# Kernel tuning notes

Hardware: AMD Instinct MI355X
Metric: run time of the kernel (lower is better)

Reference implementation:

```python
import jax, jax.numpy as jnp
import numpy as np

N = 50000          # nodes
E = 800000         # directed edges (avg degree 16)
IN_F = 1433        # Cora num_features
N_CLS = 7          # Cora num_classes
HEADS = 8
HID = 32
NEG_SLOPE = 0.2    # PyG GATConv default negative_slope


def gat_conv(x, src, dst, W, a_src, a_dst, bias, heads, out_ch):
    """PyG GATConv (concat=True, add_self_loops=True, eval mode)."""
    n = x.shape[0]
    h = (x @ W).reshape(n, heads, out_ch)            # [N, H, C]
    # add self loops (PyG default)
    loop = jnp.arange(n, dtype=src.dtype)
    src = jnp.concatenate([src, loop])
    dst = jnp.concatenate([dst, loop])
    # attention logits per edge: a_src . h_src + a_dst . h_dst
    alpha_src = (h * a_src).sum(-1)                  # [N, H]
    alpha_dst = (h * a_dst).sum(-1)                  # [N, H]
    e = jax.nn.leaky_relu(alpha_src[src] + alpha_dst[dst], NEG_SLOPE)  # [E+N, H]
    # segment softmax over incoming edges of each destination node
    m = jax.ops.segment_max(e, dst, num_segments=n)  # [N, H]
    p = jnp.exp(e - m[dst])
    denom = jax.ops.segment_sum(p, dst, num_segments=n)
    alpha = p / denom[dst]                           # [E+N, H]
    # attention-weighted scatter-aggregate of source features
    out = jax.ops.segment_sum(h[src] * alpha[:, :, None], dst, num_segments=n)  # [N, H, C]
    return out.reshape(n, heads * out_ch) + bias


def setup_inputs() -> dict:
    key = jax.random.key(0)
    ks = jax.random.split(key, 12)
    s = 0.05
    x = jax.random.normal(ks[0], (N, IN_F), dtype=jnp.float32)
    edge_index = jax.random.randint(ks[1], (2, E), 0, N, dtype=jnp.int32)
    W1 = jax.random.normal(ks[2], (IN_F, HEADS * HID), dtype=jnp.float32) * s
    att_src1 = jax.random.normal(ks[3], (HEADS, HID), dtype=jnp.float32) * s
    att_dst1 = jax.random.normal(ks[4], (HEADS, HID), dtype=jnp.float32) * s
    bias1 = jnp.zeros((HEADS * HID,), dtype=jnp.float32)
    W2 = jax.random.normal(ks[5], (HEADS * HID, HEADS * N_CLS), dtype=jnp.float32) * s
    att_src2 = jax.random.normal(ks[6], (HEADS, N_CLS), dtype=jnp.float32) * s
    att_dst2 = jax.random.normal(ks[7], (HEADS, N_CLS), dtype=jnp.float32) * s
    bias2 = jnp.zeros((HEADS * N_CLS,), dtype=jnp.float32)
    return {
        "x": x, "edge_index": edge_index,
        "W1": W1, "att_src1": att_src1, "att_dst1": att_dst1, "bias1": bias1,
        "W2": W2, "att_src2": att_src2, "att_dst2": att_dst2, "bias2": bias2,
    }


def reference(x, edge_index, W1, att_src1, att_dst1, bias1,
              W2, att_src2, att_dst2, bias2):
    src, dst = edge_index[0], edge_index[1]
    # dropout (p=0.6) is identity in eval mode
    h = gat_conv(x, src, dst, W1, att_src1, att_dst1, bias1, HEADS, HID)
    h = jax.nn.elu(h)
    out = gat_conv(h, src, dst, W2, att_src2, att_dst2, bias2, HEADS, N_CLS)
    return out  # [N, HEADS * N_CLS]
```

## Files before the change

### kernel.cpp

```cpp
#include <hip/hip_runtime.h>
#include <math.h>

typedef short s16x8 __attribute__((ext_vector_type(8)));
typedef float f32x4 __attribute__((ext_vector_type(4)));

#define SLOPE 0.2f
#define K1 1433
#define KP 1440
#define NKB 45

static __device__ __forceinline__ float leaky(float x) {
  return x > 0.f ? x : SLOPE * x;
}

static __device__ __forceinline__ unsigned short f2bf(float f) {
  unsigned u = __builtin_bit_cast(unsigned, f);
  u += 0x7FFFu + ((u >> 16) & 1u);
  return (unsigned short)(u >> 16);
}
static __device__ __forceinline__ float bf2f(unsigned short h) {
  unsigned u = ((unsigned)h) << 16;
  return __builtin_bit_cast(float, u);
}

__global__ void w1t_kernel(const float* __restrict__ W1,
                           unsigned short* __restrict__ w1f) {
  int tid = blockIdx.x * 256 + threadIdx.x;
  if (tid >= NKB * 2 * 16 * 64) return;
  int l = tid & 63;
  int chunk = tid >> 6;
  int ntg = chunk & 15;
  int hl = (chunk >> 4) & 1;
  int kb = chunk >> 5;
  int n = ntg * 16 + (l & 15);
  int kbase = kb * 32 + (l >> 4) * 8;
  unsigned short o[8];
#pragma unroll
  for (int e = 0; e < 8; ++e) {
    int k = kbase + e;
    float v = (k < K1) ? W1[(long)k * 256 + n] : 0.f;
    unsigned short h = f2bf(v);
    o[e] = hl ? f2bf(v - bf2f(h)) : h;
  }
  *(ulonglong2*)(w1f + (long)tid * 8) = *(ulonglong2*)o;
}

__global__ __launch_bounds__(256) void gemm1_mfma_kernel(
    const float* __restrict__ A, const unsigned short* __restrict__ w1f,
    float* __restrict__ C, int M) {
  __shared__ unsigned short As[2][4 * 2 * 64 * 8];
  __shared__ unsigned short Bs[2][16 * 2 * 64 * 8];
  const int t = threadIdx.x;
  const int w = t >> 6, l = t & 63;
  const int row0 = blockIdx.x * 64;

  f32x4 acc[4][4];
#pragma unroll
  for (int mt = 0; mt < 4; ++mt)
#pragma unroll
    for (int nt = 0; nt < 4; ++nt)
#pragma unroll
      for (int r = 0; r < 4; ++r) acc[mt][nt][r] = 0.f;

  const int sr = t >> 2, sg = t & 3;
  const int smt = sr >> 4, slr = sr & 15;
  const int lane_dst = slr + 16 * sg;
  const bool rowok = (row0 + sr) < M;
  const float* arow = A + (long)(row0 + sr) * K1;

  float v[8];

#pragma unroll
  for (int q = 0; q < 8; ++q) {
    int c = w * 8 + q, ng = c >> 1, hl = c & 1;
    const unsigned short* gsrc = w1f + ((((long)0 * 2 + hl) * 16 + ng) * 64 + l) * 8;
    unsigned short* ldst = &Bs[0][(ng * 2 + hl) * 512];
    __builtin_amdgcn_global_load_lds(
        (const __attribute__((address_space(1))) unsigned int*)gsrc,
        (__attribute__((address_space(3))) unsigned int*)ldst, 16, 0, 0);
  }
  {
    int kbase = sg * 8;
#pragma unroll
    for (int i = 0; i < 8; ++i) {
      int gk = kbase + i;
      v[i] = (rowok && gk < K1) ? arow[gk] : 0.f;
    }
    unsigned short hv[8], lv[8];
#pragma unroll
    for (int e = 0; e < 8; ++e) {
      unsigned short h = f2bf(v[e]);
      hv[e] = h;
      lv[e] = f2bf(v[e] - bf2f(h));
    }
    *(ulonglong2*)&As[0][((smt * 2 + 0) * 64 + lane_dst) * 8] = *(ulonglong2*)hv;
    *(ulonglong2*)&As[0][((smt * 2 + 1) * 64 + lane_dst) * 8] = *(ulonglong2*)lv;
  }
  __syncthreads();

  int cur = 0;
  for (int kb = 0; kb < NKB; ++kb) {
    const int nxt = kb + 1;
    if (nxt < NKB) {
#pragma unroll
      for (int q = 0; q < 8; ++q) {
        int c = w * 8 + q, ng = c >> 1, hl = c & 1;
        const unsigned short* gsrc =
            w1f + ((((long)nxt * 2 + hl) * 16 + ng) * 64 + l) * 8;
        unsigned short* ldst = &Bs[cur ^ 1][(ng * 2 + hl) * 512];
        __builtin_amdgcn_global_load_lds(
            (const __attribute__((address_space(1))) unsigned int*)gsrc,
            (__attribute__((address_space(3))) unsigned int*)ldst, 16, 0, 0);
      }
      int kbase = nxt * 32 + sg * 8;
#pragma unroll
      for (int i = 0; i < 8; ++i) {
        int gk = kbase + i;
        v[i] = (rowok && gk < K1) ? arow[gk] : 0.f;
      }
    }
    {
      s16x8 ah[4], al[4];
#pragma unroll
      for (int mt = 0; mt < 4; ++mt) {
        ah[mt] = *(const s16x8*)&As[cur][(mt * 2 + 0) * 512 + l * 8];
        al[mt] = *(const s16x8*)&As[cur][(mt * 2 + 1) * 512 + l * 8];
      }
#pragma unroll
      for (int nt = 0; nt < 4; ++nt) {
        int ng = w * 4 + nt;
        s16x8 bh = *(const s16x8*)&Bs[cur][(ng * 2 + 0) * 512 + l * 8];
        s16x8 bl = *(const s16x8*)&Bs[cur][(ng * 2 + 1) * 512 + l * 8];
#pragma unroll
        for (int mt = 0; mt < 4; ++mt) {
          acc[mt][nt] = __builtin_amdgcn_mfma_f32_16x16x32_bf16(
              ah[mt], bh, acc[mt][nt], 0, 0, 0);
          acc[mt][nt] = __builtin_amdgcn_mfma_f32_16x16x32_bf16(
              ah[mt], bl, acc[mt][nt], 0, 0, 0);
          acc[mt][nt] = __builtin_amdgcn_mfma_f32_16x16x32_bf16(
              al[mt], bh, acc[mt][nt], 0, 0, 0);
        }
      }
    }
    if (nxt < NKB) {
      unsigned short hv[8], lv[8];
#pragma unroll
      for (int e = 0; e < 8; ++e) {
        unsigned short h = f2bf(v[e]);
        hv[e] = h;
        lv[e] = f2bf(v[e] - bf2f(h));
      }
      *(ulonglong2*)&As[cur ^ 1][((smt * 2 + 0) * 64 + lane_dst) * 8] =
          *(ulonglong2*)hv;
      *(ulonglong2*)&As[cur ^ 1][((smt * 2 + 1) * 64 + lane_dst) * 8] =
          *(ulonglong2*)lv;
      __syncthreads();
    }
    cur ^= 1;
  }
  const int crow4 = (l >> 4) * 4;
  const int ccol = l & 15;
#pragma unroll
  for (int mt = 0; mt < 4; ++mt) {
#pragma unroll
    for (int r = 0; r < 4; ++r) {
      int grow = row0 + mt * 16 + crow4 + r;
      if (grow < M) {
#pragma unroll
        for (int nt = 0; nt < 4; ++nt) {
          int gcol = w * 64 + nt * 16 + ccol;
          C[(long)grow * 256 + gcol] = acc[mt][nt][r];
        }
      }
    }
  }
}

__global__ void alpha1_kernel(const float* __restrict__ h1,
    const float* __restrict__ a_src, const float* __restrict__ a_dst,
    float* __restrict__ as_o, float* __restrict__ ad_o, int N) {
  int i = blockIdx.x * blockDim.x + threadIdx.x;
  if (i >= N * 8) return;
  int h = i & 7;
  const float* hp = h1 + (long)(i >> 3) * 256 + h * 32;
  const float* sp = a_src + h * 32;
  const float* dp = a_dst + h * 32;
  float s1 = 0.f, s2 = 0.f;
#pragma unroll
  for (int c = 0; c < 32; c += 4) {
    float4 v = *(const float4*)(hp + c);
    float4 ws = *(const float4*)(sp + c);
    float4 wd = *(const float4*)(dp + c);
    s1 += v.x * ws.x + v.y * ws.y + v.z * ws.z + v.w * ws.w;
    s2 += v.x * wd.x + v.y * wd.y + v.z * wd.z + v.w * wd.w;
  }
  as_o[i] = s1;
  ad_o[i] = s2;
}

__global__ void hist_kernel(const int* __restrict__ dst, int* __restrict__ cnt,
                            int E, int N) {
  int e = blockIdx.x * blockDim.x + threadIdx.x;
  if (e >= E + N) return;
  int d = (e < E) ? dst[e] : (e - E);
  atomicAdd(&cnt[d], 1);
}

__global__ __launch_bounds__(1024) void scan_kernel(
    const int* __restrict__ cnt, int* __restrict__ rowptr,
    int* __restrict__ cursor, int N) {
  __shared__ int part[1024];
  const int tid = threadIdx.x;
  const int chunk = (N + 1023) / 1024;
  const int base = tid * chunk;
  const int lim = min(base + chunk, N);
  int sum = 0;
  for (int i = base; i < lim; ++i) sum += cnt[i];
  part[tid] = sum;
  __syncthreads();
  for (int off = 1; off < 1024; off <<= 1) {
    int v = (tid >= off) ? part[tid - off] : 0;
    __syncthreads();
    part[tid] += v;
    __syncthreads();
  }
  int run = (tid == 0) ? 0 : part[tid - 1];
  for (int i = base; i < lim; ++i) {
    rowptr[i] = run;
    cursor[i] = run;
    run += cnt[i];
  }
  if (tid == 1023) rowptr[N] = part[1023];
}

__global__ void scatter_kernel(const int* __restrict__ src,
    const int* __restrict__ dst, int* __restrict__ cursor,
    int* __restrict__ csr_src, int E, int N) {
  int e = blockIdx.x * blockDim.x + threadIdx.x;
  if (e >= E + N) return;
  int s, d;
  if (e < E) { s = src[e]; d = dst[e]; } else { s = e - E; d = s; }
  int pos = atomicAdd(&cursor[d], 1);
  csr_src[pos] = s;
}

__global__ __launch_bounds__(256) void agg1_fused_kernel(
    const int* __restrict__ rowptr, const int* __restrict__ csr_src,
    const float* __restrict__ as_, const float* __restrict__ ad_,
    const float* __restrict__ h1, const float* __restrict__ bias,
    float* __restrict__ act, int N) {
  int d = blockIdx.x * 4 + (threadIdx.x >> 6);
  if (d >= N) return;
  int l = threadIdx.x & 63;
  int h = l >> 3;
  int rs = rowptr[d], re = rowptr[d + 1];
  float adv = ad_[d * 8 + h];
  float4 acc = make_float4(0.f, 0.f, 0.f, 0.f);
  float den = 0.f;
  for (int i = rs; i < re; ++i) {
    int s = csr_src[i];
    float a = __expf(leaky(as_[s * 8 + h] + adv));
    den += a;
    float4 v = *(const float4*)(h1 + (long)s * 256 + l * 4);
    acc.x += a * v.x; acc.y += a * v.y; acc.z += a * v.z; acc.w += a * v.w;
  }
  float inv = 1.f / den;
  float4 b = *(const float4*)(bias + l * 4);
  float4 o;
  o.x = acc.x * inv + b.x; o.y = acc.y * inv + b.y;
  o.z = acc.z * inv + b.z; o.w = acc.w * inv + b.w;
  o.x = o.x > 0.f ? o.x : expm1f(o.x);
  o.y = o.y > 0.f ? o.y : expm1f(o.y);
  o.z = o.z > 0.f ? o.z : expm1f(o.z);
  o.w = o.w > 0.f ? o.w : expm1f(o.w);
  *(float4*)(act + (long)d * 256 + l * 4) = o;
}

__global__ __launch_bounds__(256) void gemm2_kernel(const float* __restrict__ act,
    const float* __restrict__ W2, const float* __restrict__ a_src2,
    const float* __restrict__ a_dst2, float* __restrict__ h2,
    float* __restrict__ as_o, float* __restrict__ ad_o, int N) {
  __shared__ float Ws[256 * 56];
  for (int i = threadIdx.x; i < 256 * 56; i += 256) Ws[i] = W2[i];
  __syncthreads();
  int n = blockIdx.x * 32 + (threadIdx.x >> 3);
  int h = threadIdx.x & 7;
  if (n >= N) return;
  const float* ap = act + (long)n * 256;
  float acc[7] = {0.f, 0.f, 0.f, 0.f, 0.f, 0.f, 0.f};
  for (int k0 = 0; k0 < 256; k0 += 4) {
    float4 a = *(const float4*)(ap + k0);
    float av[4] = {a.x, a.y, a.z, a.w};
#pragma unroll
    for (int kk = 0; kk < 4; ++kk) {
      const float* wp = &Ws[(k0 + kk) * 56 + h * 7];
#pragma unroll
      for (int j = 0; j < 7; ++j) acc[j] += av[kk] * wp[j];
    }
  }
  float* hp = h2 + (long)n * 56 + h * 7;
  float s1 = 0.f, s2 = 0.f;
#pragma unroll
  for (int j = 0; j < 7; ++j) {
    hp[j] = acc[j];
    s1 += acc[j] * a_src2[h * 7 + j];
    s2 += acc[j] * a_dst2[h * 7 + j];
  }
  as_o[n * 8 + h] = s1;
  ad_o[n * 8 + h] = s2;
}

__global__ __launch_bounds__(256) void agg2_fused_kernel(
    const int* __restrict__ rowptr, const int* __restrict__ csr_src,
    const float* __restrict__ as_, const float* __restrict__ ad_,
    const float* __restrict__ h2, const float* __restrict__ bias,
    float* __restrict__ out, int N) {
  int d = blockIdx.x * 4 + (threadIdx.x >> 6);
  if (d >= N) return;
  int l = threadIdx.x & 63;
  int h = l >> 3, j = l & 7;
  int rs = rowptr[d], re = rowptr[d + 1];
  float adv = ad_[d * 8 + h];
  float acc = 0.f, den = 0.f;
  for (int i = rs; i < re; ++i) {
    int s = csr_src[i];
    float a = __expf(leaky(as_[s * 8 + h] + adv));
    den += a;
    if (j < 7) acc += a * h2[(long)s * 56 + h * 7 + j];
  }
  if (j < 7) out[(long)d * 56 + h * 7 + j] = acc / den + bias[h * 7 + j];
}

extern "C" void kernel_launch(void* const* d_in, const int* in_sizes, int n_in,
                              void* d_out, int out_size, void* d_ws, size_t ws_size,
                              hipStream_t stream) {
  const float* x    = (const float*)d_in[0];
  const int*   ei   = (const int*)d_in[1];
  const float* W1   = (const float*)d_in[2];
  const float* asr1 = (const float*)d_in[3];
  const float* adt1 = (const float*)d_in[4];
  const float* b1   = (const float*)d_in[5];
  const float* W2   = (const float*)d_in[6];
  const float* asr2 = (const float*)d_in[7];
  const float* adt2 = (const float*)d_in[8];
  const float* b2   = (const float*)d_in[9];
  float* out = (float*)d_out;

  const int N = in_sizes[0] / K1;
  const int E = in_sizes[1] / 2;
  const int* src = ei;
  const int* dst = ei + E;

  float* ws = (float*)d_ws;
  float* h1  = ws; ws += (long)N * 256;
  float* act = ws; ws += (long)N * 256;
  float* h2  = ws; ws += (long)N * 56;
  float* as1 = ws; ws += N * 8;
  float* ad1 = ws; ws += N * 8;
  float* as2 = ws; ws += N * 8;
  float* ad2 = ws; ws += N * 8;
  unsigned short* w1f = (unsigned short*)ws; ws += NKB * 2 * 16 * 64 * 8 / 2;
  int* cnt     = (int*)ws; ws += N;
  int* rowptr  = (int*)ws; ws += N + 1;
  int* cursor  = (int*)ws; ws += N;
  int* csr_src = (int*)ws; ws += E + N;

  hipMemsetAsync(cnt, 0, (size_t)N * sizeof(int), stream);

  dim3 blk(256);

  hist_kernel<<<dim3((E + N + 255) / 256), blk, 0, stream>>>(dst, cnt, E, N);
  scan_kernel<<<dim3(1), dim3(1024), 0, stream>>>(cnt, rowptr, cursor, N);
  scatter_kernel<<<dim3((E + N + 255) / 256), blk, 0, stream>>>(
      src, dst, cursor, csr_src, E, N);
  {
    int tot = NKB * 2 * 16 * 64;
    w1t_kernel<<<dim3((tot + 255) / 256), blk, 0, stream>>>(W1, w1f);
  }

  gemm1_mfma_kernel<<<dim3((N + 63) / 64), blk, 0, stream>>>(x, w1f, h1, N);
  alpha1_kernel<<<dim3((N * 8 + 255) / 256), blk, 0, stream>>>(h1, asr1, adt1, as1, ad1, N);
  agg1_fused_kernel<<<dim3((N + 3) / 4), blk, 0, stream>>>(
      rowptr, csr_src, as1, ad1, h1, b1, act, N);
  gemm2_kernel<<<dim3((N + 31) / 32), blk, 0, stream>>>(act, W2, asr2, adt2, h2, as2, ad2, N);
  agg2_fused_kernel<<<dim3((N + 3) / 4), blk, 0, stream>>>(
      rowptr, csr_src, as2, ad2, h2, b2, out, N);
}
```

Baseline: 742.6 us.

## Drop W1 low-bf16 split term and gather bf16 features in aggregation

```diff
diff --git a/kernel.cpp b/kernel.cpp
--- a/kernel.cpp
+++ b/kernel.cpp
@@ -26,12 +26,11 @@
 __global__ void w1t_kernel(const float* __restrict__ W1,
                            unsigned short* __restrict__ w1f) {
   int tid = blockIdx.x * 256 + threadIdx.x;
-  if (tid >= NKB * 2 * 16 * 64) return;
+  if (tid >= NKB * 16 * 64) return;
   int l = tid & 63;
   int chunk = tid >> 6;
   int ntg = chunk & 15;
-  int hl = (chunk >> 4) & 1;
-  int kb = chunk >> 5;
+  int kb = chunk >> 4;
   int n = ntg * 16 + (l & 15);
   int kbase = kb * 32 + (l >> 4) * 8;
   unsigned short o[8];
@@ -39,17 +38,16 @@
   for (int e = 0; e < 8; ++e) {
     int k = kbase + e;
     float v = (k < K1) ? W1[(long)k * 256 + n] : 0.f;
-    unsigned short h = f2bf(v);
-    o[e] = hl ? f2bf(v - bf2f(h)) : h;
+    o[e] = f2bf(v);
   }
   *(ulonglong2*)(w1f + (long)tid * 8) = *(ulonglong2*)o;
 }
 
-__global__ __launch_bounds__(256) void gemm1_mfma_kernel(
+__global__ __launch_bounds__(256, 3) void gemm1_mfma_kernel(
     const float* __restrict__ A, const unsigned short* __restrict__ w1f,
     float* __restrict__ C, int M) {
   __shared__ unsigned short As[2][4 * 2 * 64 * 8];
-  __shared__ unsigned short Bs[2][16 * 2 * 64 * 8];
+  __shared__ unsigned short Bs[2][16 * 64 * 8];
   const int t = threadIdx.x;
   const int w = t >> 6, l = t & 63;
   const int row0 = blockIdx.x * 64;
@@ -71,10 +69,10 @@
   float v[8];
 
 #pragma unroll
-  for (int q = 0; q < 8; ++q) {
-    int c = w * 8 + q, ng = c >> 1, hl = c & 1;
-    const unsigned short* gsrc = w1f + ((((long)0 * 2 + hl) * 16 + ng) * 64 + l) * 8;
-    unsigned short* ldst = &Bs[0][(ng * 2 + hl) * 512];
+  for (int q = 0; q < 4; ++q) {
+    int ng = w * 4 + q;
+    const unsigned short* gsrc = w1f + (((long)0 * 16 + ng) * 64 + l) * 8;
+    unsigned short* ldst = &Bs[0][ng * 512];
     __builtin_amdgcn_global_load_lds(
         (const __attribute__((address_space(1))) unsigned int*)gsrc,
         (__attribute__((address_space(3))) unsigned int*)ldst, 16, 0, 0);
@@ -103,11 +101,11 @@
     const int nxt = kb + 1;
     if (nxt < NKB) {
 #pragma unroll
-      for (int q = 0; q < 8; ++q) {
-        int c = w * 8 + q, ng = c >> 1, hl = c & 1;
+      for (int q = 0; q < 4; ++q) {
+        int ng = w * 4 + q;
         const unsigned short* gsrc =
-            w1f + ((((long)nxt * 2 + hl) * 16 + ng) * 64 + l) * 8;
-        unsigned short* ldst = &Bs[cur ^ 1][(ng * 2 + hl) * 512];
+            w1f + (((long)nxt * 16 + ng) * 64 + l) * 8;
+        unsigned short* ldst = &Bs[cur ^ 1][ng * 512];
         __builtin_amdgcn_global_load_lds(
             (const __attribute__((address_space(1))) unsigned int*)gsrc,
             (__attribute__((address_space(3))) unsigned int*)ldst, 16, 0, 0);
@@ -120,27 +118,24 @@
       }
     }
     {
-      s16x8 ah[4], al[4];
+      s16x8 ah[4], al[4], bh[4];
 #pragma unroll
       for (int mt = 0; mt < 4; ++mt) {
         ah[mt] = *(const s16x8*)&As[cur][(mt * 2 + 0) * 512 + l * 8];
         al[mt] = *(const s16x8*)&As[cur][(mt * 2 + 1) * 512 + l * 8];
       }
 #pragma unroll
-      for (int nt = 0; nt < 4; ++nt) {
-        int ng = w * 4 + nt;
-        s16x8 bh = *(const s16x8*)&Bs[cur][(ng * 2 + 0) * 512 + l * 8];
-        s16x8 bl = *(const s16x8*)&Bs[cur][(ng * 2 + 1) * 512 + l * 8];
+      for (int nt = 0; nt < 4; ++nt)
+        bh[nt] = *(const s16x8*)&Bs[cur][(w * 4 + nt) * 512 + l * 8];
+#pragma unroll
+      for (int nt = 0; nt < 4; ++nt)
 #pragma unroll
         for (int mt = 0; mt < 4; ++mt) {
           acc[mt][nt] = __builtin_amdgcn_mfma_f32_16x16x32_bf16(
-              ah[mt], bh, acc[mt][nt], 0, 0, 0);
+              ah[mt], bh[nt], acc[mt][nt], 0, 0, 0);
           acc[mt][nt] = __builtin_amdgcn_mfma_f32_16x16x32_bf16(
-              ah[mt], bl, acc[mt][nt], 0, 0, 0);
-          acc[mt][nt] = __builtin_amdgcn_mfma_f32_16x16x32_bf16(
-              al[mt], bh, acc[mt][nt], 0, 0, 0);
+              al[mt], bh[nt], acc[mt][nt], 0, 0, 0);
         }
-      }
     }
     if (nxt < NKB) {
       unsigned short hv[8], lv[8];
@@ -178,13 +173,15 @@
 
 __global__ void alpha1_kernel(const float* __restrict__ h1,
     const float* __restrict__ a_src, const float* __restrict__ a_dst,
-    float* __restrict__ as_o, float* __restrict__ ad_o, int N) {
+    float* __restrict__ as_o, float* __restrict__ ad_o,
+    unsigned short* __restrict__ h1b, int N) {
   int i = blockIdx.x * blockDim.x + threadIdx.x;
   if (i >= N * 8) return;
   int h = i & 7;
   const float* hp = h1 + (long)(i >> 3) * 256 + h * 32;
   const float* sp = a_src + h * 32;
   const float* dp = a_dst + h * 32;
+  unsigned short ob[32];
   float s1 = 0.f, s2 = 0.f;
 #pragma unroll
   for (int c = 0; c < 32; c += 4) {
@@ -193,9 +190,15 @@
     float4 wd = *(const float4*)(dp + c);
     s1 += v.x * ws.x + v.y * ws.y + v.z * ws.z + v.w * ws.w;
     s2 += v.x * wd.x + v.y * wd.y + v.z * wd.z + v.w * wd.w;
+    ob[c] = f2bf(v.x); ob[c + 1] = f2bf(v.y);
+    ob[c + 2] = f2bf(v.z); ob[c + 3] = f2bf(v.w);
   }
   as_o[i] = s1;
   ad_o[i] = s2;
+  unsigned short* op = h1b + (long)(i >> 3) * 256 + h * 32;
+#pragma unroll
+  for (int c = 0; c < 32; c += 8)
+    *(ulonglong2*)(op + c) = *(ulonglong2*)(ob + c);
 }
 
 __global__ void hist_kernel(const int* __restrict__ dst, int* __restrict__ cnt,
@@ -247,7 +250,7 @@
 __global__ __launch_bounds__(256) void agg1_fused_kernel(
     const int* __restrict__ rowptr, const int* __restrict__ csr_src,
     const float* __restrict__ as_, const float* __restrict__ ad_,
-    const float* __restrict__ h1, const float* __restrict__ bias,
+    const unsigned short* __restrict__ h1b, const float* __restrict__ bias,
     float* __restrict__ act, int N) {
   int d = blockIdx.x * 4 + (threadIdx.x >> 6);
   if (d >= N) return;
@@ -261,8 +264,9 @@
     int s = csr_src[i];
     float a = __expf(leaky(as_[s * 8 + h] + adv));
     den += a;
-    float4 v = *(const float4*)(h1 + (long)s * 256 + l * 4);
-    acc.x += a * v.x; acc.y += a * v.y; acc.z += a * v.z; acc.w += a * v.w;
+    ushort4 u = *(const ushort4*)(h1b + (long)s * 256 + l * 4);
+    acc.x += a * bf2f(u.x); acc.y += a * bf2f(u.y);
+    acc.z += a * bf2f(u.z); acc.w += a * bf2f(u.w);
   }
   float inv = 1.f / den;
   float4 b = *(const float4*)(bias + l * 4);
@@ -278,7 +282,7 @@
 
 __global__ __launch_bounds__(256) void gemm2_kernel(const float* __restrict__ act,
     const float* __restrict__ W2, const float* __restrict__ a_src2,
-    const float* __restrict__ a_dst2, float* __restrict__ h2,
+    const float* __restrict__ a_dst2, unsigned short* __restrict__ h2b,
     float* __restrict__ as_o, float* __restrict__ ad_o, int N) {
   __shared__ float Ws[256 * 56];
   for (int i = threadIdx.x; i < 256 * 56; i += 256) Ws[i] = W2[i];
@@ -298,11 +302,11 @@
       for (int j = 0; j < 7; ++j) acc[j] += av[kk] * wp[j];
     }
   }
-  float* hp = h2 + (long)n * 56 + h * 7;
+  unsigned short* hp = h2b + (long)n * 56 + h * 7;
   float s1 = 0.f, s2 = 0.f;
 #pragma unroll
   for (int j = 0; j < 7; ++j) {
-    hp[j] = acc[j];
+    hp[j] = f2bf(acc[j]);
     s1 += acc[j] * a_src2[h * 7 + j];
     s2 += acc[j] * a_dst2[h * 7 + j];
   }
@@ -313,7 +317,7 @@
 __global__ __launch_bounds__(256) void agg2_fused_kernel(
     const int* __restrict__ rowptr, const int* __restrict__ csr_src,
     const float* __restrict__ as_, const float* __restrict__ ad_,
-    const float* __restrict__ h2, const float* __restrict__ bias,
+    const unsigned short* __restrict__ h2b, const float* __restrict__ bias,
     float* __restrict__ out, int N) {
   int d = blockIdx.x * 4 + (threadIdx.x >> 6);
   if (d >= N) return;
@@ -326,7 +330,7 @@
     int s = csr_src[i];
     float a = __expf(leaky(as_[s * 8 + h] + adv));
     den += a;
-    if (j < 7) acc += a * h2[(long)s * 56 + h * 7 + j];
+    if (j < 7) acc += a * bf2f(h2b[(long)s * 56 + h * 7 + j]);
   }
   if (j < 7) out[(long)d * 56 + h * 7 + j] = acc / den + bias[h * 7 + j];
 }
@@ -354,12 +358,13 @@
   float* ws = (float*)d_ws;
   float* h1  = ws; ws += (long)N * 256;
   float* act = ws; ws += (long)N * 256;
-  float* h2  = ws; ws += (long)N * 56;
   float* as1 = ws; ws += N * 8;
   float* ad1 = ws; ws += N * 8;
   float* as2 = ws; ws += N * 8;
   float* ad2 = ws; ws += N * 8;
-  unsigned short* w1f = (unsigned short*)ws; ws += NKB * 2 * 16 * 64 * 8 / 2;
+  unsigned short* h1b = (unsigned short*)ws; ws += (long)N * 128;
+  unsigned short* h2b = (unsigned short*)ws; ws += (long)N * 28;
+  unsigned short* w1f = (unsigned short*)ws; ws += NKB * 16 * 64 * 8 / 2;
   int* cnt     = (int*)ws; ws += N;
   int* rowptr  = (int*)ws; ws += N + 1;
   int* cursor  = (int*)ws; ws += N;
@@ -374,15 +379,17 @@
   scatter_kernel<<<dim3((E + N + 255) / 256), blk, 0, stream>>>(
       src, dst, cursor, csr_src, E, N);
   {
-    int tot = NKB * 2 * 16 * 64;
+    int tot = NKB * 16 * 64;
     w1t_kernel<<<dim3((tot + 255) / 256), blk, 0, stream>>>(W1, w1f);
   }
 
   gemm1_mfma_kernel<<<dim3((N + 63) / 64), blk, 0, stream>>>(x, w1f, h1, N);
-  alpha1_kernel<<<dim3((N * 8 + 255) / 256), blk, 0, stream>>>(h1, asr1, adt1, as1, ad1, N);
+  alpha1_kernel<<<dim3((N * 8 + 255) / 256), blk, 0, stream>>>(
+      h1, asr1, adt1, as1, ad1, h1b, N);
   agg1_fused_kernel<<<dim3((N + 3) / 4), blk, 0, stream>>>(
-      rowptr, csr_src, as1, ad1, h1, b1, act, N);
-  gemm2_kernel<<<dim3((N + 31) / 32), blk, 0, stream>>>(act, W2, asr2, adt2, h2, as2, ad2, N);
+      rowptr, csr_src, as1, ad1, h1b, b1, act, N);
+  gemm2_kernel<<<dim3((N + 31) / 32), blk, 0, stream>>>(
+      act, W2, asr2, adt2, h2b, as2, ad2, N);
   agg2_fused_kernel<<<dim3((N + 3) / 4), blk, 0, stream>>>(
-      rowptr, csr_src, as2, ad2, h2, b2, out, N);
-}
+      rowptr, csr_src, as2, ad2, h2b, b2, out, N);
+}
```

New measurement: 727.1 us. -2.1%, faster.
